# Performance work log

Measured on AMD Instinct MI355X. Metric: run time of the kernel, lower is better.

## Reference

```python
import jax, jax.numpy as jnp
import numpy as np

H = 16  # num_heads
THETA = 10000.0


def _rope(x, position):
    # x: (B, H, N, hd), position: (B, N) float
    B, h, N, hd = x.shape
    freqs = 1.0 / (THETA ** (jnp.arange(0, hd, 2, dtype=jnp.float32) / hd))  # (hd/2,)
    ang = position[:, None, :, None] * freqs  # (B, 1, N, hd/2)
    cos, sin = jnp.cos(ang), jnp.sin(ang)
    xr = x.reshape(B, h, N, hd // 2, 2)
    re, im = xr[..., 0], xr[..., 1]
    out_re = re * cos - im * sin
    out_im = re * sin + im * cos
    return jnp.stack([out_re, out_im], axis=-1).reshape(B, h, N, hd)


def setup_inputs() -> dict:
    key = jax.random.key(0)
    ks = jax.random.split(key, 6)
    B, N, D = 4, 2049, 1024
    x = jax.random.normal(ks[0], (B, N, D), dtype=jnp.float32)
    position = jnp.sort(jax.random.randint(ks[1], (B, N - 1), 0, 8192), axis=-1).astype(jnp.int32)
    w_qkv = jax.random.normal(ks[2], (3 * D, D), dtype=jnp.float32) * (1.0 / np.sqrt(D))
    b_qkv = jax.random.normal(ks[3], (3 * D,), dtype=jnp.float32) * 0.02
    w_fc = jax.random.normal(ks[4], (D, D), dtype=jnp.float32) * (1.0 / np.sqrt(D))
    b_fc = jax.random.normal(ks[5], (D,), dtype=jnp.float32) * 0.02
    return {"x": x, "position": position, "w_qkv": w_qkv, "b_qkv": b_qkv, "w_fc": w_fc, "b_fc": b_fc}


def reference(x, position, w_qkv, b_qkv, w_fc, b_fc):
    B, N, D = x.shape
    hd = D // H
    # fused QKV projection
    qkv = x @ w_qkv.T + b_qkv                      # (B, N, 3D)
    qkv = qkv.reshape(B, N, 3, H, hd)
    qkv = jnp.transpose(qkv, (2, 0, 3, 1, 4))       # (3, B, H, N, hd)
    q, k, v = qkv[0], qkv[1], qkv[2]
    # rotary on non-cls tokens, cls passthrough
    pos_f = position.astype(jnp.float32)
    q = jnp.concatenate([q[:, :, :1, :], _rope(q[:, :, 1:, :], pos_f)], axis=2)
    k = jnp.concatenate([k[:, :, :1, :], _rope(k[:, :, 1:, :], pos_f)], axis=2)
    # SDPA (no causal mask, eval mode -> no dropout)
    scale = 1.0 / jnp.sqrt(jnp.float32(hd))
    scores = jnp.einsum('bhqd,bhkd->bhqk', q, k) * scale
    attn = jax.nn.softmax(scores, axis=-1)
    out = jnp.einsum('bhqk,bhkd->bhqd', attn, v)    # (B, H, N, hd)
    out = jnp.transpose(out, (0, 2, 1, 3)).reshape(B, N, D)
    out = out @ w_fc.T + b_fc
    return out
```

## Files before the change

### kernel.cpp

```cpp
#include <hip/hip_runtime.h>

typedef unsigned short u16;
typedef __attribute__((ext_vector_type(8))) _Float16 f16x8;
typedef __attribute__((ext_vector_type(4))) float f32x4;

#define MFMAH(a, b, c) __builtin_amdgcn_mfma_f32_16x16x32_f16((a), (b), (c), 0, 0, 0)

__device__ __forceinline__ u16 f2h(float f) {
  _Float16 h = (_Float16)f;
  return __builtin_bit_cast(u16, h);
}
__device__ __forceinline__ float h2f(u16 h) {
  return (float)__builtin_bit_cast(_Float16, h);
}
__device__ __forceinline__ unsigned pk_h(float a, float b) {
  return (unsigned)f2h(a) | ((unsigned)f2h(b) << 16);
}
__device__ __forceinline__ unsigned pkrtz(float a, float b) {
  unsigned r;
  asm("v_cvt_pkrtz_f16_f32 %0, %1, %2" : "=v"(r) : "v"(a), "v"(b));
  return r;
}

__global__ void prep_cast(const float* __restrict__ x, u16* __restrict__ xh,
                          const float* __restrict__ wqf, u16* __restrict__ wq,
                          const float* __restrict__ wff, u16* __restrict__ wf,
                          long nx, long nq, long nf) {
  long total = nx + nq + nf;
  long stride = (long)gridDim.x * blockDim.x;
  for (long i = (long)blockIdx.x * blockDim.x + threadIdx.x; i < total; i += stride) {
    const float4* src;
    ushort4* dst;
    long j;
    if (i < nx) { src = (const float4*)x; dst = (ushort4*)xh; j = i; }
    else if (i < nx + nq) { src = (const float4*)wqf; dst = (ushort4*)wq; j = i - nx; }
    else { src = (const float4*)wff; dst = (ushort4*)wf; j = i - nx - nq; }
    float4 v = src[j];
    ushort4 h;
    h.x = f2h(v.x); h.y = f2h(v.y); h.z = f2h(v.z); h.w = f2h(v.w);
    dst[j] = h;
  }
}

__global__ void cs_table_kernel(const int* __restrict__ pos, float2* __restrict__ cst) {
  int idx = blockIdx.x * 256 + threadIdx.x;
  int i = idx & 31;
  int r = idx >> 5;
  int ti = r & 2047;
  int b = r >> 11;
  int p = pos[b * 2048 + ti];
  float fr = (float)pow(10000.0, -(double)i / 32.0);
  float angf = (float)p * fr;
  double sd, cd;
  sincos((double)angf, &sd, &cd);
  cst[idx] = make_float2((float)cd, (float)sd);
}

__global__ void kpad_kernel(u16* __restrict__ kh, int N, int NP) {
  const int per_bh = (NP - N) * 32;
  int idx = blockIdx.x * 256 + threadIdx.x;
  if (idx >= 64 * per_bh) return;
  int bh = idx / per_bh, r = idx - bh * per_bh;
  size_t u = (((size_t)bh * NP + N) * 64 >> 1) + r;
  ((unsigned*)kh)[u] = 0;
}

__global__ __launch_bounds__(256) void vtransT_kernel(const u16* __restrict__ vb_,
                                                      u16* __restrict__ ot, int N, int NP) {
  __shared__ u16 tile[64][72];
  const int bh = blockIdx.y;
  const int t0 = blockIdx.x * 64;
  const u16* ih = vb_ + (size_t)bh * N * 64;
#pragma unroll
  for (int p = 0; p < 4; ++p) {
    int idx = p * 256 + threadIdx.x;
    int tloc = idx >> 4, c = (idx & 15) * 4;
    int t = t0 + tloc;
    ushort4 a = make_ushort4(0, 0, 0, 0);
    if (t < N) a = *(const ushort4*)(ih + (size_t)t * 64 + c);
    *(ushort4*)&tile[tloc][c] = a;
  }
  __syncthreads();
  u16* oh = ot + (size_t)bh * 64 * NP;
#pragma unroll
  for (int p = 0; p < 4; ++p) {
    int idx = p * 256 + threadIdx.x;
    int d = idx >> 4, tq = (idx & 15) * 4;
    int t = t0 + tq;
    if (t < NP) {
      ushort4 a;
      a.x = tile[tq + 0][d]; a.y = tile[tq + 1][d];
      a.z = tile[tq + 2][d]; a.w = tile[tq + 3][d];
      *(ushort4*)(oh + (size_t)d * NP + t) = a;
    }
  }
}

__device__ __forceinline__ int swz_off(int R, int lg) {
  return R * 32 + ((lg ^ ((R >> 1) & 3)) << 3);
}
__device__ __forceinline__ void stage_tile(const u16* __restrict__ g, u16* l,
                                           int row0, int rmax, int K, int k0, int tid) {
#pragma unroll
  for (int t = 0; t < 2; ++t) {
    int c = t * 256 + tid;
    int row = c >> 2;
    int kc = (((c & 3) ^ ((c >> 3) & 3)) << 3);
    int gr = row0 + row;
    if (gr > rmax) gr = rmax;
    const u16* gp = g + (size_t)gr * K + (k0 + kc);
    __builtin_amdgcn_global_load_lds((const __attribute__((address_space(1))) void*)gp,
                                     (__attribute__((address_space(3))) void*)(l + c * 8),
                                     16, 0, 0);
  }
}

template <int EPI>
__global__ __launch_bounds__(256) void gemm_s1(
    const u16* __restrict__ Aw, const u16* __restrict__ Bw,
    const float* __restrict__ bias, const float2* __restrict__ cst,
    float* __restrict__ outf,
    u16* __restrict__ oq, u16* __restrict__ ok, u16* __restrict__ ov,
    int M, int Nn, int K, int Ntok, int NP) {
  __shared__ u16 A0[4096], B0[4096], A1[4096], B1[4096];
  const int tid = threadIdx.x;
  const int wid = tid >> 6, lane = tid & 63;
  const int wm = wid >> 1, wn = wid & 1;
  const int lg = lane >> 4, lm = lane & 15;
  const int id = blockIdx.x;
  const int chunk = (int)gridDim.x >> 3, nx = Nn >> 7;
  const int swz = (id & 7) * chunk + (id >> 3);
  const int mbase = (swz / nx) * 128, nbase = (swz % nx) * 128;

  f32x4 acc[4][4];
  const f32x4 zero = {0.f, 0.f, 0.f, 0.f};
#pragma unroll
  for (int a = 0; a < 4; ++a)
#pragma unroll
    for (int b = 0; b < 4; ++b) acc[a][b] = zero;

  stage_tile(Aw, A0, mbase, M - 1, K, 0, tid);
  stage_tile(Bw, B0, nbase, Nn - 1, K, 0, tid);
  __syncthreads();

  for (int k0 = 0; k0 < K; k0 += 64) {
    if (k0 + 32 < K) {
      stage_tile(Aw, A1, mbase, M - 1, K, k0 + 32, tid);
      stage_tile(Bw, B1, nbase, Nn - 1, K, k0 + 32, tid);
    }
    {
      f16x8 a[4], w[4];
#pragma unroll
      for (int f = 0; f < 4; ++f) {
        a[f] = *(const f16x8*)&A0[swz_off(wm * 64 + f * 16 + lm, lg)];
        w[f] = *(const f16x8*)&B0[swz_off(wn * 64 + f * 16 + lm, lg)];
      }
#pragma unroll
      for (int fm = 0; fm < 4; ++fm)
#pragma unroll
        for (int fn = 0; fn < 4; ++fn) acc[fm][fn] = MFMAH(a[fm], w[fn], acc[fm][fn]);
    }
    __syncthreads();
    if (k0 + 64 < K) {
      stage_tile(Aw, A0, mbase, M - 1, K, k0 + 64, tid);
      stage_tile(Bw, B0, nbase, Nn - 1, K, k0 + 64, tid);
    }
    {
      f16x8 a[4], w[4];
#pragma unroll
      for (int f = 0; f < 4; ++f) {
        a[f] = *(const f16x8*)&A1[swz_off(wm * 64 + f * 16 + lm, lg)];
        w[f] = *(const f16x8*)&B1[swz_off(wn * 64 + f * 16 + lm, lg)];
      }
#pragma unroll
      for (int fm = 0; fm < 4; ++fm)
#pragma unroll
        for (int fn = 0; fn < 4; ++fn) acc[fm][fn] = MFMAH(a[fm], w[fn], acc[fm][fn]);
    }
    __syncthreads();
  }

  const int which = (EPI == 0) ? (nbase >> 10) : 1;
  const bool odd = (lm & 1);
#pragma unroll
  for (int fm = 0; fm < 4; ++fm)
#pragma unroll
    for (int fn = 0; fn < 4; ++fn) {
      int col = nbase + wn * 64 + fn * 16 + lm;
      float bv = bias[col];
      int h2 = (col >> 6) & 15, d2 = col & 63;
#pragma unroll
      for (int i = 0; i < 4; ++i) {
        int row = mbase + wm * 64 + fm * 16 + lg * 4 + i;
        float v = acc[fm][fn][i] + bv;
        float partner = __shfl_xor(v, 1);
        if (row < M) {
          if (EPI == 1) {
            outf[(size_t)row * Nn + col] = v;
          } else {
            int b2 = row / Ntok, t2 = row - b2 * Ntok;
            int bh2 = b2 * 16 + h2;
            if (which == 2) {
              ov[((size_t)bh2 * Ntok + t2) * 64 + d2] = f2h(v);
            } else {
              float out = v;
              if (t2 > 0) {
                float2 cs = cst[((size_t)(b2 << 11) + (t2 - 1)) * 32 + (d2 >> 1)];
                out = v * cs.x + (odd ? partner * cs.y : -partner * cs.y);
              }
              if (which == 0) {
                out *= 0.18033688011112042f;
                oq[((size_t)bh2 * Ntok + t2) * 64 + d2] = f2h(out);
              } else {
                ok[((size_t)bh2 * NP + t2) * 64 + d2] = f2h(out);
              }
            }
          }
        }
      }
    }
}

template <bool DO_STAGE, bool TAIL>
__device__ __forceinline__ void attn_tile(
    int kv0, int kvn,
    const u16* Kc, const u16* Vc, u16* Kn, u16* Vn,
    const u16* kgb, const u16* vgb,
    int tid, int lg, int lm, int kvbase,
    const f16x8 (&qf16)[2][2],
    float (&m_)[2], float (&l_)[2], f32x4 (&oacc)[2][4],
    unsigned (*pexw)[64][4], int N) {
  if (DO_STAGE) {
    __builtin_amdgcn_global_load_lds(
        (const __attribute__((address_space(1))) void*)(kgb + (size_t)kvn * 64),
        (__attribute__((address_space(3))) void*)(Kn + tid * 8), 16, 0, 0);
    __builtin_amdgcn_global_load_lds(
        (const __attribute__((address_space(1))) void*)(vgb + kvn),
        (__attribute__((address_space(3))) void*)(Vn + tid * 8), 16, 0, 0);
  }

  const f32x4 zero = {0.f, 0.f, 0.f, 0.f};
  f32x4 s[2][4];
#pragma unroll
  for (int qf = 0; qf < 2; ++qf)
#pragma unroll
    for (int cf = 0; cf < 4; ++cf) s[qf][cf] = zero;
#pragma unroll
  for (int cf = 0; cf < 4; ++cf)
#pragma unroll
    for (int dk = 0; dk < 2; ++dk) {
      f16x8 kf = *(const f16x8*)&Kc[kvbase + dk * 2048 + cf * 128];
      s[0][cf] = MFMAH(kf, qf16[0][dk], s[0][cf]);
      s[1][cf] = MFMAH(kf, qf16[1][dk], s[1][cf]);
    }
  if (TAIL) {
#pragma unroll
    for (int qf = 0; qf < 2; ++qf)
#pragma unroll
      for (int cf = 0; cf < 4; ++cf)
#pragma unroll
        for (int i = 0; i < 4; ++i)
          if (kv0 + cf * 16 + lg * 4 + i >= N) s[qf][cf][i] = -1e30f;
  }

  unsigned us[2][8];
#pragma unroll
  for (int qf = 0; qf < 2; ++qf) {
    float mx = s[qf][0][0];
#pragma unroll
    for (int cf = 0; cf < 4; ++cf)
#pragma unroll
      for (int i = 0; i < 4; ++i) mx = fmaxf(mx, s[qf][cf][i]);
    mx = fmaxf(mx, __shfl_xor(mx, 16));
    mx = fmaxf(mx, __shfl_xor(mx, 32));
    float mr = m_[qf];
    bool nore = __all(mx - mr <= 8.f) != 0;
    float mnew = nore ? mr : fmaxf(mr, mx);
    float p[16];
#pragma unroll
    for (int cf = 0; cf < 4; ++cf)
#pragma unroll
      for (int i = 0; i < 4; ++i)
        p[cf * 4 + i] = __builtin_amdgcn_exp2f(s[qf][cf][i] - mnew);
    float ps = 0.f;
#pragma unroll
    for (int j = 0; j < 16; ++j) ps += p[j];
    ps += __shfl_xor(ps, 16);
    ps += __shfl_xor(ps, 32);
    if (nore) {
      l_[qf] += ps;
    } else {
      float sc = __builtin_amdgcn_exp2f(mr - mnew);
      l_[qf] = l_[qf] * sc + ps;
      m_[qf] = mnew;
#pragma unroll
      for (int c = 0; c < 4; ++c)
#pragma unroll
        for (int i = 0; i < 4; ++i) oacc[qf][c][i] *= sc;
    }
#pragma unroll
    for (int w = 0; w < 8; ++w) us[qf][w] = pkrtz(p[2 * w], p[2 * w + 1]);
  }

  f16x8 pb[2][2];
  const int ga = (lg & 1) * 2, gb = ga + 1;
  const int cfs2 = (lg >> 1) * 2;
  const int prow = lg * 16 + lm;
#pragma unroll
  for (int ks = 0; ks < 2; ++ks) {
    *(uint4*)&pexw[0][prow][0] =
        make_uint4(us[0][ks * 4], us[0][ks * 4 + 1], us[0][ks * 4 + 2], us[0][ks * 4 + 3]);
    *(uint4*)&pexw[1][prow][0] =
        make_uint4(us[1][ks * 4], us[1][ks * 4 + 1], us[1][ks * 4 + 2], us[1][ks * 4 + 3]);
#pragma unroll
    for (int qf = 0; qf < 2; ++qf) {
      uint2 r0 = *(const uint2*)&pexw[qf][ga * 16 + lm][cfs2];
      uint2 r1 = *(const uint2*)&pexw[qf][gb * 16 + lm][cfs2];
      uint4 pu = make_uint4(r0.x, r0.y, r1.x, r1.y);
      pb[qf][ks] = __builtin_bit_cast(f16x8, pu);
    }
  }

#pragma unroll
  for (int c = 0; c < 4; ++c)
#pragma unroll
    for (int ks = 0; ks < 2; ++ks) {
      f16x8 vh = *(const f16x8*)&Vc[kvbase + ks * 2048 + c * 128];
      oacc[0][c] = MFMAH(vh, pb[0][ks], oacc[0][c]);
      oacc[1][c] = MFMAH(vh, pb[1][ks], oacc[1][c]);
    }
}

__global__ __launch_bounds__(512, 4) void attn_kernel(
    const u16* __restrict__ qh, const u16* __restrict__ kh, const u16* __restrict__ vth,
    u16* __restrict__ outh, int N, int NP) {
  __shared__ u16 K0[4096], V0[4096], K1[4096], V1[4096];
  __shared__ unsigned pexm[8][2][64][4];

  const int id = blockIdx.x;
  const int swz = (id & 7) * 72 + (id >> 3);
  const int qblk = swz % 9;
  const int bh = swz / 9;
  const int b = bh >> 4, h = bh & 15;
  const int tid = threadIdx.x;
  const int wid = tid >> 6, lane = tid & 63;
  const int lg = lane >> 4, lm = lane & 15;
  const int qbase = qblk * 256 + wid * 32;
  const size_t qoff = (size_t)bh * N * 64;
  const size_t koff = (size_t)bh * NP * 64;
  const size_t voff = (size_t)bh * 64 * NP;

  const int jK = tid & 63, rK = tid >> 6;
  const u16* kgb = kh + koff + (size_t)jK * 64 + rK * 8;
  const u16* vgb = vth + voff + (size_t)jK * NP + rK * 8;
  const int kvbase = lg * 512 + lm * 8;

  f16x8 qf16[2][2];
#pragma unroll
  for (int qf = 0; qf < 2; ++qf) {
    int qr = qbase + qf * 16 + lm;
    if (qr > N - 1) qr = N - 1;
    const u16* qp = qh + qoff + (size_t)qr * 64 + lg * 8;
    qf16[qf][0] = *(const f16x8*)(qp);
    qf16[qf][1] = *(const f16x8*)(qp + 32);
  }

  const f32x4 zero = {0.f, 0.f, 0.f, 0.f};
  f32x4 oacc[2][4];
#pragma unroll
  for (int qf = 0; qf < 2; ++qf)
#pragma unroll
    for (int c = 0; c < 4; ++c) oacc[qf][c] = zero;
  float m_[2] = {-1e30f, -1e30f}, l_[2] = {0.f, 0.f};
  unsigned(*pexw)[64][4] = pexm[wid];

  __builtin_amdgcn_global_load_lds(
      (const __attribute__((address_space(1))) void*)kgb,
      (__attribute__((address_space(3))) void*)(K0 + tid * 8), 16, 0, 0);
  __builtin_amdgcn_global_load_lds(
      (const __attribute__((address_space(1))) void*)vgb,
      (__attribute__((address_space(3))) void*)(V0 + tid * 8), 16, 0, 0);
  asm volatile("s_waitcnt vmcnt(0)" ::: "memory");
  __builtin_amdgcn_s_barrier();

  for (int t = 0; t < 32; t += 2) {
    attn_tile<true, false>(t * 64, (t + 1) * 64, K0, V0, K1, V1, kgb, vgb,
                           tid, lg, lm, kvbase, qf16, m_, l_, oacc, pexw, N);
    asm volatile("s_waitcnt vmcnt(0)" ::: "memory");
    __builtin_amdgcn_s_barrier();
    attn_tile<true, false>((t + 1) * 64, (t + 2) * 64, K1, V1, K0, V0, kgb, vgb,
                           tid, lg, lm, kvbase, qf16, m_, l_, oacc, pexw, N);
    asm volatile("s_waitcnt vmcnt(0)" ::: "memory");
    __builtin_amdgcn_s_barrier();
  }
  attn_tile<false, true>(32 * 64, 0, K0, V0, K1, V1, kgb, vgb,
                         tid, lg, lm, kvbase, qf16, m_, l_, oacc, pexw, N);

#pragma unroll
  for (int qf = 0; qf < 2; ++qf) {
    int t = qbase + qf * 16 + lm;
    if (t < N) {
      float rl = 1.f / l_[qf];
      size_t rowoff = ((size_t)(b * N + t)) * 1024 + h * 64 + lg * 4;
#pragma unroll
      for (int c = 0; c < 4; ++c) {
        float v0 = oacc[qf][c][0] * rl, v1 = oacc[qf][c][1] * rl;
        float v2 = oacc[qf][c][2] * rl, v3 = oacc[qf][c][3] * rl;
        unsigned hh01 = pk_h(v0, v1), hh23 = pk_h(v2, v3);
        *(uint2*)(outh + rowoff + c * 16) = make_uint2(hh01, hh23);
      }
    }
  }
}

extern "C" void kernel_launch(void* const* d_in, const int* in_sizes, int n_in,
                              void* d_out, int out_size, void* d_ws, size_t ws_size,
                              hipStream_t stream) {
  const float* x     = (const float*)d_in[0];
  const int*   pos   = (const int*)  d_in[1];
  const float* w_qkv = (const float*)d_in[2];
  const float* b_qkv = (const float*)d_in[3];
  const float* w_fc  = (const float*)d_in[4];
  const float* b_fc  = (const float*)d_in[5];
  (void)in_sizes; (void)n_in; (void)out_size; (void)ws_size;

  const int B = 4, N = 2049, NP = 2112;
  const long EL = (long)B * N * 1024;
  const long ELP = (long)B * 16 * NP * 64;

  char* base = (char*)d_ws;
  size_t off = 0;
  auto alloc = [&](size_t bytes) -> void* {
    void* p = base + off;
    off += (bytes + 255) & ~(size_t)255;
    return p;
  };
  u16* qhh = (u16*)alloc(EL * 2);
  u16* khh = (u16*)alloc(ELP * 2);
  u16* vbh = (u16*)alloc(EL * 2);
  u16* vth = (u16*)alloc((size_t)64 * 64 * NP * 2);
  u16* xh  = (u16*)alloc(EL * 2);
  u16* wq  = (u16*)alloc((size_t)3072 * 1024 * 2);
  u16* wf  = (u16*)alloc((size_t)1024 * 1024 * 2);
  float2* cst = (float2*)alloc((size_t)B * 2048 * 32 * 8);

  prep_cast<<<2048, 256, 0, stream>>>(x, xh, w_qkv, wq, w_fc, wf,
                                      EL / 4, (long)3072 * 1024 / 4, (long)1024 * 1024 / 4);
  cs_table_kernel<<<(B * 2048 * 32) / 256, 256, 0, stream>>>(pos, cst);
  gemm_s1<0><<<dim3(1560), 256, 0, stream>>>(xh, wq, b_qkv, cst, nullptr,
                                             qhh, khh, vbh, 8196, 3072, 1024, N, NP);
  kpad_kernel<<<(64 * (NP - N) * 32 + 255) / 256, 256, 0, stream>>>(khh, N, NP);
  vtransT_kernel<<<dim3(NP / 64, 64), 256, 0, stream>>>(vbh, vth, N, NP);
  attn_kernel<<<dim3(576), 512, 0, stream>>>(qhh, khh, vth, xh, N, NP);
  gemm_s1<1><<<dim3(520), 256, 0, stream>>>(xh, wf, b_fc, nullptr,
                                            (float*)d_out, nullptr, nullptr, nullptr,
                                            8196, 1024, 1024, N, NP);
}
```

Before: 343.0 us.

## Split attention KV range across two blocks and merge with combine kernel

Splits each attention work item's 33 KV tiles into two halves handled by separate blocks, doubling the grid from 576 to 1152. Each half writes normalized partial outputs plus (max, sum) stats, which a new combine kernel merges with log-sum-exp weights into the projection input. The change also reorganizes the P exchange so it runs per query fragment, halving the shared-memory exchange buffer. The aim is better occupancy and load balance on the many CUs, paid for with an extra kernel launch and extra global traffic for the partials.

```diff
diff --git a/kernel.cpp b/kernel.cpp
--- a/kernel.cpp
+++ b/kernel.cpp
@@ -229,7 +229,7 @@
     int tid, int lg, int lm, int kvbase,
     const f16x8 (&qf16)[2][2],
     float (&m_)[2], float (&l_)[2], f32x4 (&oacc)[2][4],
-    unsigned (*pexw)[64][4], int N) {
+    unsigned (*pexw)[4], int N) {
   if (DO_STAGE) {
     __builtin_amdgcn_global_load_lds(
         (const __attribute__((address_space(1))) void*)(kgb + (size_t)kvn * 64),
@@ -263,7 +263,10 @@
           if (kv0 + cf * 16 + lg * 4 + i >= N) s[qf][cf][i] = -1e30f;
   }
 
-  unsigned us[2][8];
+  f16x8 pb[2][2];
+  const int ga = (lg & 1) * 2, gb = ga + 1;
+  const int cfs2 = (lg >> 1) * 2;
+  const int prow = lg * 16 + lm;
 #pragma unroll
   for (int qf = 0; qf < 2; ++qf) {
     float mx = s[qf][0][0];
@@ -298,24 +301,15 @@
 #pragma unroll
         for (int i = 0; i < 4; ++i) oacc[qf][c][i] *= sc;
     }
-#pragma unroll
-    for (int w = 0; w < 8; ++w) us[qf][w] = pkrtz(p[2 * w], p[2 * w + 1]);
-  }
-
-  f16x8 pb[2][2];
-  const int ga = (lg & 1) * 2, gb = ga + 1;
-  const int cfs2 = (lg >> 1) * 2;
-  const int prow = lg * 16 + lm;
-#pragma unroll
-  for (int ks = 0; ks < 2; ++ks) {
-    *(uint4*)&pexw[0][prow][0] =
-        make_uint4(us[0][ks * 4], us[0][ks * 4 + 1], us[0][ks * 4 + 2], us[0][ks * 4 + 3]);
-    *(uint4*)&pexw[1][prow][0] =
-        make_uint4(us[1][ks * 4], us[1][ks * 4 + 1], us[1][ks * 4 + 2], us[1][ks * 4 + 3]);
-#pragma unroll
-    for (int qf = 0; qf < 2; ++qf) {
-      uint2 r0 = *(const uint2*)&pexw[qf][ga * 16 + lm][cfs2];
-      uint2 r1 = *(const uint2*)&pexw[qf][gb * 16 + lm][cfs2];
+    unsigned us[8];
+#pragma unroll
+    for (int w = 0; w < 8; ++w) us[w] = pkrtz(p[2 * w], p[2 * w + 1]);
+#pragma unroll
+    for (int ks = 0; ks < 2; ++ks) {
+      *(uint4*)&pexw[prow][0] =
+          make_uint4(us[ks * 4], us[ks * 4 + 1], us[ks * 4 + 2], us[ks * 4 + 3]);
+      uint2 r0 = *(const uint2*)&pexw[ga * 16 + lm][cfs2];
+      uint2 r1 = *(const uint2*)&pexw[gb * 16 + lm][cfs2];
       uint4 pu = make_uint4(r0.x, r0.y, r1.x, r1.y);
       pb[qf][ks] = __builtin_bit_cast(f16x8, pu);
     }
@@ -333,15 +327,16 @@
 
 __global__ __launch_bounds__(512, 4) void attn_kernel(
     const u16* __restrict__ qh, const u16* __restrict__ kh, const u16* __restrict__ vth,
-    u16* __restrict__ outh, int N, int NP) {
+    u16* __restrict__ opart, float2* __restrict__ ml, int N, int NP) {
   __shared__ u16 K0[4096], V0[4096], K1[4096], V1[4096];
-  __shared__ unsigned pexm[8][2][64][4];
+  __shared__ unsigned pexm[8][64][4];
 
   const int id = blockIdx.x;
-  const int swz = (id & 7) * 72 + (id >> 3);
-  const int qblk = swz % 9;
-  const int bh = swz / 9;
-  const int b = bh >> 4, h = bh & 15;
+  const int swz = (id & 7) * 144 + (id >> 3);
+  const int part = swz & 1;
+  const int rest = swz >> 1;
+  const int qblk = rest % 9;
+  const int bh = rest / 9;
   const int tid = threadIdx.x;
   const int wid = tid >> 6, lane = tid & 63;
   const int lg = lane >> 4, lm = lane & 15;
@@ -349,6 +344,7 @@
   const size_t qoff = (size_t)bh * N * 64;
   const size_t koff = (size_t)bh * NP * 64;
   const size_t voff = (size_t)bh * 64 * NP;
+  const int t_lo = part ? 17 : 0, t_hi = part ? 33 : 17;
 
   const int jK = tid & 63, rK = tid >> 6;
   const u16* kgb = kh + koff + (size_t)jK * 64 + rK * 8;
@@ -372,45 +368,82 @@
 #pragma unroll
     for (int c = 0; c < 4; ++c) oacc[qf][c] = zero;
   float m_[2] = {-1e30f, -1e30f}, l_[2] = {0.f, 0.f};
-  unsigned(*pexw)[64][4] = pexm[wid];
+  unsigned(*pexw)[4] = &pexm[wid][0];
 
   __builtin_amdgcn_global_load_lds(
-      (const __attribute__((address_space(1))) void*)kgb,
+      (const __attribute__((address_space(1))) void*)(kgb + (size_t)(t_lo * 64) * 64),
       (__attribute__((address_space(3))) void*)(K0 + tid * 8), 16, 0, 0);
   __builtin_amdgcn_global_load_lds(
-      (const __attribute__((address_space(1))) void*)vgb,
+      (const __attribute__((address_space(1))) void*)(vgb + t_lo * 64),
       (__attribute__((address_space(3))) void*)(V0 + tid * 8), 16, 0, 0);
   asm volatile("s_waitcnt vmcnt(0)" ::: "memory");
   __builtin_amdgcn_s_barrier();
 
-  for (int t = 0; t < 32; t += 2) {
-    attn_tile<true, false>(t * 64, (t + 1) * 64, K0, V0, K1, V1, kgb, vgb,
+  u16 *Kc = K0, *Vc = V0, *Kn = K1, *Vn = V1;
+  for (int t = t_lo; t < t_hi - 1; ++t) {
+    attn_tile<true, false>(t * 64, (t + 1) * 64, Kc, Vc, Kn, Vn, kgb, vgb,
                            tid, lg, lm, kvbase, qf16, m_, l_, oacc, pexw, N);
     asm volatile("s_waitcnt vmcnt(0)" ::: "memory");
     __builtin_amdgcn_s_barrier();
-    attn_tile<true, false>((t + 1) * 64, (t + 2) * 64, K1, V1, K0, V0, kgb, vgb,
+    u16* tk = Kc; Kc = Kn; Kn = tk;
+    u16* tv = Vc; Vc = Vn; Vn = tv;
+  }
+  if (part)
+    attn_tile<false, true>((t_hi - 1) * 64, 0, Kc, Vc, Kn, Vn, kgb, vgb,
                            tid, lg, lm, kvbase, qf16, m_, l_, oacc, pexw, N);
-    asm volatile("s_waitcnt vmcnt(0)" ::: "memory");
-    __builtin_amdgcn_s_barrier();
-  }
-  attn_tile<false, true>(32 * 64, 0, K0, V0, K1, V1, kgb, vgb,
-                         tid, lg, lm, kvbase, qf16, m_, l_, oacc, pexw, N);
+  else
+    attn_tile<false, false>((t_hi - 1) * 64, 0, Kc, Vc, Kn, Vn, kgb, vgb,
+                            tid, lg, lm, kvbase, qf16, m_, l_, oacc, pexw, N);
 
 #pragma unroll
   for (int qf = 0; qf < 2; ++qf) {
     int t = qbase + qf * 16 + lm;
     if (t < N) {
       float rl = 1.f / l_[qf];
-      size_t rowoff = ((size_t)(b * N + t)) * 1024 + h * 64 + lg * 4;
+      size_t rowo = (((size_t)part * 64 + bh) * 2304 + t) * 64 + lg * 4;
 #pragma unroll
       for (int c = 0; c < 4; ++c) {
         float v0 = oacc[qf][c][0] * rl, v1 = oacc[qf][c][1] * rl;
         float v2 = oacc[qf][c][2] * rl, v3 = oacc[qf][c][3] * rl;
-        unsigned hh01 = pk_h(v0, v1), hh23 = pk_h(v2, v3);
-        *(uint2*)(outh + rowoff + c * 16) = make_uint2(hh01, hh23);
+        *(uint2*)(opart + rowo + c * 16) = make_uint2(pk_h(v0, v1), pk_h(v2, v3));
       }
-    }
-  }
+      if (lg == 0) ml[((size_t)part * 64 + bh) * 2304 + t] = make_float2(m_[qf], l_[qf]);
+    }
+  }
+}
+
+__global__ __launch_bounds__(256) void combine_kernel(const u16* __restrict__ opart,
+                                                      const float2* __restrict__ ml,
+                                                      u16* __restrict__ xh, int N) {
+  int idx = blockIdx.x * 256 + threadIdx.x;
+  int r = idx >> 3;
+  if (r >= 64 * N) return;
+  int d8 = (idx & 7) * 8;
+  int bh = r / N, t = r - bh * N;
+  float2 mlA = ml[(size_t)bh * 2304 + t];
+  float2 mlB = ml[(size_t)(64 + bh) * 2304 + t];
+  float M = fmaxf(mlA.x, mlB.x);
+  float wA = mlA.y * __builtin_amdgcn_exp2f(mlA.x - M);
+  float wB = mlB.y * __builtin_amdgcn_exp2f(mlB.x - M);
+  float inv = 1.f / (wA + wB);
+  wA *= inv; wB *= inv;
+  const u16* pA = opart + ((size_t)bh * 2304 + t) * 64 + d8;
+  const u16* pB = opart + ((size_t)(64 + bh) * 2304 + t) * 64 + d8;
+  ushort4 a0 = *(const ushort4*)pA, a1 = *(const ushort4*)(pA + 4);
+  ushort4 b0 = *(const ushort4*)pB, b1 = *(const ushort4*)(pB + 4);
+  ushort4 o0, o1;
+  o0.x = f2h(wA * h2f(a0.x) + wB * h2f(b0.x));
+  o0.y = f2h(wA * h2f(a0.y) + wB * h2f(b0.y));
+  o0.z = f2h(wA * h2f(a0.z) + wB * h2f(b0.z));
+  o0.w = f2h(wA * h2f(a0.w) + wB * h2f(b0.w));
+  o1.x = f2h(wA * h2f(a1.x) + wB * h2f(b1.x));
+  o1.y = f2h(wA * h2f(a1.y) + wB * h2f(b1.y));
+  o1.z = f2h(wA * h2f(a1.z) + wB * h2f(b1.z));
+  o1.w = f2h(wA * h2f(a1.w) + wB * h2f(b1.w));
+  int b = bh >> 4, h = bh & 15;
+  u16* dst = xh + ((size_t)(b * N + t)) * 1024 + h * 64 + d8;
+  *(ushort4*)dst = o0;
+  *(ushort4*)(dst + 4) = o1;
 }
 
 extern "C" void kernel_launch(void* const* d_in, const int* in_sizes, int n_in,
@@ -443,6 +476,8 @@
   u16* wq  = (u16*)alloc((size_t)3072 * 1024 * 2);
   u16* wf  = (u16*)alloc((size_t)1024 * 1024 * 2);
   float2* cst = (float2*)alloc((size_t)B * 2048 * 32 * 8);
+  u16* opart = (u16*)alloc((size_t)2 * 64 * 2304 * 64 * 2);
+  float2* ml = (float2*)alloc((size_t)2 * 64 * 2304 * 8);
 
   prep_cast<<<2048, 256, 0, stream>>>(x, xh, w_qkv, wq, w_fc, wf,
                                       EL / 4, (long)3072 * 1024 / 4, (long)1024 * 1024 / 4);
@@ -451,7 +486,8 @@
                                              qhh, khh, vbh, 8196, 3072, 1024, N, NP);
   kpad_kernel<<<(64 * (NP - N) * 32 + 255) / 256, 256, 0, stream>>>(khh, N, NP);
   vtransT_kernel<<<dim3(NP / 64, 64), 256, 0, stream>>>(vbh, vth, N, NP);
-  attn_kernel<<<dim3(576), 512, 0, stream>>>(qhh, khh, vth, xh, N, NP);
+  attn_kernel<<<dim3(1152), 512, 0, stream>>>(qhh, khh, vth, opart, ml, N, NP);
+  combine_kernel<<<dim3((64 * N * 8 + 255) / 256), 256, 0, stream>>>(opart, ml, xh, N);
   gemm_s1<1><<<dim3(520), 256, 0, stream>>>(xh, wf, b_fc, nullptr,
                                             (float*)d_out, nullptr, nullptr, nullptr,
                                             8196, 1024, 1024, N, NP);
```

Measured after the change: 355.5 us. +3.6%, slower.
